# Optimization experiments

Measured on AMD Instinct MI355X. Metric: run time of the kernel, lower is better.

The kernel has to match this reference:

```python
import jax, jax.numpy as jnp
import numpy as np


def setup_inputs() -> dict:
    key = jax.random.key(0)
    B, S, D, H = 4, 2048, 1024, 16
    hd = D // H
    ks = jax.random.split(key, 11)
    sc = 1.0 / np.sqrt(D)
    return {
        "keys": jax.random.normal(ks[0], (B, S, D), jnp.float32),
        "queries": jax.random.normal(ks[1], (B, S, D), jnp.float32),
        "values": jax.random.normal(ks[2], (B, S, D), jnp.float32),
        "Wq": jax.random.normal(ks[3], (H, D, hd), jnp.float32) * sc,
        "bq": jax.random.normal(ks[4], (H, hd), jnp.float32) * 0.02,
        "Wk": jax.random.normal(ks[5], (H, D, hd), jnp.float32) * sc,
        "bk": jax.random.normal(ks[6], (H, hd), jnp.float32) * 0.02,
        "Wv": jax.random.normal(ks[7], (H, D, hd), jnp.float32) * sc,
        "bv": jax.random.normal(ks[8], (H, hd), jnp.float32) * 0.02,
        "Wo": jax.random.normal(ks[9], (D, D), jnp.float32) * sc,
        "bo": jax.random.normal(ks[10], (D,), jnp.float32) * 0.02,
    }


def reference(keys, queries, values, Wq, bq, Wk, bk, Wv, bv, Wo, bo):
    # Per-head linear projections: [B,S,D] x [H,D,hd] -> [B,H,S,hd]
    q = jnp.einsum("bsd,hde->bhse", queries, Wq) + bq[None, :, None, :]
    k = jnp.einsum("bsd,hde->bhse", keys, Wk) + bk[None, :, None, :]
    v = jnp.einsum("bsd,hde->bhse", values, Wv) + bv[None, :, None, :]

    hd = q.shape[-1]
    S = q.shape[2]
    scores = jnp.einsum("bhse,bhte->bhst", q, k) / jnp.sqrt(jnp.float32(hd))
    causal = jnp.tril(jnp.ones((S, S), dtype=bool))  # tril buffer
    scores = jnp.where(causal[None, None, :, :], scores, -jnp.inf)
    attn = jax.nn.softmax(scores, axis=-1)  # dropout p=0 (eval)

    o = jnp.einsum("bhst,bhte->bhse", attn, v)  # [B,H,S,hd]
    # concat heads -> [B,S,H*hd]
    o = o.transpose(0, 2, 1, 3).reshape(o.shape[0], S, -1)
    return o @ Wo + bo
```

## Files before the change

### kernel.cpp

```cpp
#include <hip/hip_runtime.h>
#include <stdint.h>

typedef unsigned short u16;
typedef __attribute__((ext_vector_type(4))) float f32x4;
typedef __attribute__((ext_vector_type(8))) short bfrag;

static __device__ __forceinline__ u16 f2bf(float f) {
  union { float f; uint32_t u; } v; v.f = f;
  return (u16)((v.u + 0x7fffu + ((v.u >> 16) & 1u)) >> 16);
}
static __device__ __forceinline__ uint32_t cvtpk(float lo, float hi) {
  uint32_t r;
  asm("v_cvt_pk_bf16_f32 %0, %1, %2" : "=v"(r) : "v"(lo), "v"(hi));
  return r;
}
static __device__ __forceinline__ uint32_t pk2bf(float lo, float hi) {
  union { float f; uint32_t u; } a, b; a.f = lo; b.f = hi;
  return __builtin_amdgcn_perm(b.u + 0x8000u, a.u + 0x8000u, 0x07060302u);
}

#define GLOAD16(gp, lp)                                              \
  __builtin_amdgcn_global_load_lds(                                  \
      (const __attribute__((address_space(1))) uint32_t*)(gp),       \
      (__attribute__((address_space(3))) uint32_t*)(lp), 16, 0, 0)

__global__ __launch_bounds__(256) void pack_w_hde(const float* __restrict__ W,
                                                  u16* __restrict__ Wt) {
  __shared__ float tile[64][65];
  const int h = blockIdx.y, k0 = blockIdx.x * 64;
  const int tid = threadIdx.x;
#pragma unroll
  for (int j = 0; j < 4; ++j) {
    int idx = tid + j * 256;
    int rr = idx >> 4, c4 = (idx & 15) * 4;
    const float4 v = *(const float4*)(W + (size_t)h * 65536 + (size_t)(k0 + rr) * 64 + c4);
    tile[rr][c4 + 0] = v.x; tile[rr][c4 + 1] = v.y;
    tile[rr][c4 + 2] = v.z; tile[rr][c4 + 3] = v.w;
  }
  __syncthreads();
#pragma unroll
  for (int j = 0; j < 4; ++j) {
    int idx = tid + j * 256;
    int ee = idx >> 4, c4 = (idx & 15) * 4;
    uint2 u;
    u.x = f2bf(tile[c4 + 0][ee]) | ((uint32_t)f2bf(tile[c4 + 1][ee]) << 16);
    u.y = f2bf(tile[c4 + 2][ee]) | ((uint32_t)f2bf(tile[c4 + 3][ee]) << 16);
    *(uint2*)(Wt + (size_t)(h * 64 + ee) * 1024 + k0 + c4) = u;
  }
}

__global__ __launch_bounds__(256) void transpose_w(const float* __restrict__ W,
                                                   u16* __restrict__ Wt) {
  __shared__ float tile[64][65];
  const int k0 = blockIdx.x * 64, n0 = blockIdx.y * 64;
  const int tid = threadIdx.x;
#pragma unroll
  for (int j = 0; j < 4; ++j) {
    int idx = tid + j * 256;
    int rr = idx >> 4, c4 = (idx & 15) * 4;
    const float4 v = *(const float4*)(W + (size_t)(k0 + rr) * 1024 + n0 + c4);
    tile[rr][c4 + 0] = v.x; tile[rr][c4 + 1] = v.y;
    tile[rr][c4 + 2] = v.z; tile[rr][c4 + 3] = v.w;
  }
  __syncthreads();
#pragma unroll
  for (int j = 0; j < 4; ++j) {
    int idx = tid + j * 256;
    int ee = idx >> 4, c4 = (idx & 15) * 4;
    uint2 u;
    u.x = f2bf(tile[c4 + 0][ee]) | ((uint32_t)f2bf(tile[c4 + 1][ee]) << 16);
    u.y = f2bf(tile[c4 + 2][ee]) | ((uint32_t)f2bf(tile[c4 + 3][ee]) << 16);
    *(uint2*)(Wt + (size_t)(n0 + ee) * 1024 + k0 + c4) = u;
  }
}

__global__ __launch_bounds__(256) void conv_bf16(const float* __restrict__ q,
                                                 const float* __restrict__ k,
                                                 const float* __restrict__ v,
                                                 u16* __restrict__ oq,
                                                 u16* __restrict__ ok,
                                                 u16* __restrict__ ov) {
  const float* in = (blockIdx.y == 0) ? q : (blockIdx.y == 1) ? k : v;
  u16* out = (blockIdx.y == 0) ? oq : (blockIdx.y == 1) ? ok : ov;
  const size_t i = ((size_t)blockIdx.x * 256 + threadIdx.x) * 8;
  const float4 f0 = *(const float4*)(in + i);
  const float4 f1 = *(const float4*)(in + i + 4);
  uint4 u;
  u.x = pk2bf(f0.x, f0.y); u.y = pk2bf(f0.z, f0.w);
  u.z = pk2bf(f1.x, f1.y); u.w = pk2bf(f1.z, f1.w);
  *(uint4*)(out + i) = u;
}

__global__ __launch_bounds__(256) void gemm_qkvb(
    const u16* __restrict__ cq, const u16* __restrict__ ck,
    const u16* __restrict__ cv, const u16* __restrict__ Bt,
    const float* __restrict__ bq, const float* __restrict__ bk,
    const float* __restrict__ bv,
    u16* __restrict__ Qb, u16* __restrict__ Kb, u16* __restrict__ Vt) {
  __shared__ u16 As[2][128 * 32];
  __shared__ u16 Bs[2][128 * 32];
  const int tid = threadIdx.x;
  const int n = blockIdx.x;
  const int xcd = n & 7, j = n >> 3;
  const int mb = xcd * 8 + (j & 7);
  const int nb = j >> 3;
  const int chunk = nb >> 3;
  const u16* Abf = (chunk == 0) ? cq : (chunk == 1) ? ck : cv;
  const int wid = tid >> 6, lane = tid & 63;
  const int wr = wid >> 1, wc = wid & 1;
  const int g = lane >> 4, l15 = lane & 15;
  f32x4 acc[4][4] = {};

  const int bsrc = ((lane & 3) ^ ((lane >> 3) & 3)) * 8;
  const int swzr = (l15 >> 1) & 3;
  const u16* Bg = Bt + (size_t)(nb * 128 + 2 * wid * 16 + (lane >> 2)) * 1024 + bsrc;
  const u16* Ag = Abf + (size_t)(mb * 128 + 2 * wid * 16 + (lane >> 2)) * 1024 + bsrc;

#pragma unroll
  for (int c = 0; c < 2; ++c) {
    GLOAD16(Ag + (size_t)c * 16 * 1024, &As[0][2 * wid * 512 + c * 512]);
    GLOAD16(Bg + (size_t)c * 16 * 1024, &Bs[0][2 * wid * 512 + c * 512]);
  }
  __syncthreads();
  int cur = 0;
  for (int kk = 0; kk < 32; ++kk) {
    if (kk < 31) {
      const int kn = (kk + 1) * 32;
#pragma unroll
      for (int c = 0; c < 2; ++c) {
        GLOAD16(Ag + (size_t)c * 16 * 1024 + kn, &As[cur ^ 1][2 * wid * 512 + c * 512]);
        GLOAD16(Bg + (size_t)c * 16 * 1024 + kn, &Bs[cur ^ 1][2 * wid * 512 + c * 512]);
      }
    }
    bfrag a[4], b[4];
#pragma unroll
    for (int m = 0; m < 4; ++m)
      a[m] = __builtin_bit_cast(bfrag,
          *(const uint4*)&As[cur][(wr * 64 + m * 16 + l15) * 32 + ((g ^ swzr)) * 8]);
#pragma unroll
    for (int nn = 0; nn < 4; ++nn)
      b[nn] = __builtin_bit_cast(bfrag,
          *(const uint4*)&Bs[cur][(wc * 64 + nn * 16 + l15) * 32 + ((g ^ swzr)) * 8]);
    __builtin_amdgcn_s_setprio(1);
#pragma unroll
    for (int m = 0; m < 4; ++m)
#pragma unroll
      for (int nn = 0; nn < 4; ++nn)
        acc[m][nn] = __builtin_amdgcn_mfma_f32_16x16x32_bf16(a[m], b[nn], acc[m][nn], 0, 0, 0);
    __builtin_amdgcn_s_setprio(0);
    if (kk < 31) { __syncthreads(); cur ^= 1; }
  }

  const int row0 = mb * 128 + wr * 64 + g * 4;
  const int cc0 = (nb & 7) * 128 + wc * 64 + l15;
  const float* bias = (chunk == 0) ? bq : (chunk == 1) ? bk : bv;
  const float qs = (chunk == 0) ? 0.125f : 1.0f;
#pragma unroll
  for (int m = 0; m < 4; ++m) {
#pragma unroll
    for (int nn = 0; nn < 4; ++nn) {
      const int row = row0 + m * 16;
      const int cc = cc0 + nn * 16;
      const float bcv = bias[cc];
      if (chunk < 2) {
        u16* dst = (chunk == 0) ? Qb : Kb;
#pragma unroll
        for (int r = 0; r < 4; ++r)
          dst[(size_t)(row + r) * 1024 + cc] = f2bf((acc[m][nn][r] + bcv) * qs);
      } else {
        u16 w[4];
#pragma unroll
        for (int r = 0; r < 4; ++r) w[r] = f2bf(acc[m][nn][r] + bcv);
        const size_t dst =
            ((size_t)((row >> 11) * 16 + (cc >> 6)) * 64 + (cc & 63)) * 2048 + (row & 2047);
        *(uint2*)(Vt + dst) = *(const uint2*)w;
      }
    }
  }
}

__global__ __launch_bounds__(256) void gemm_qkv(
    const float* __restrict__ Aq, const float* __restrict__ Ak,
    const float* __restrict__ Avv, const u16* __restrict__ Bt,
    const float* __restrict__ bq, const float* __restrict__ bk,
    const float* __restrict__ bv,
    u16* __restrict__ Qb, u16* __restrict__ Kb, u16* __restrict__ Vt) {
  __shared__ u16 As[2][128 * 32];
  __shared__ u16 Bs[2][128 * 32];
  const int tid = threadIdx.x;
  const int n = blockIdx.x;
  const int xcd = n & 7, j = n >> 3;
  const int mb = xcd * 8 + (j & 7);
  const int nb = j >> 3;
  const int chunk = nb >> 3;
  const float* Af = (chunk == 0) ? Aq : (chunk == 1) ? Ak : Avv;
  const int wid = tid >> 6, lane = tid & 63;
  const int wr = wid >> 1, wc = wid & 1;
  const int g = lane >> 4, l15 = lane & 15;
  f32x4 acc[4][4] = {};

  const int bsrc = ((lane & 3) ^ ((lane >> 3) & 3)) * 8;
  const u16* Bg = Bt + (size_t)(nb * 128 + 2 * wid * 16 + (lane >> 2)) * 1024 + bsrc;
  const float* Ap = Af + (size_t)(mb * 128 + (tid >> 2)) * 1024 + (tid & 3) * 8;
  const int arow = tid >> 2;
  const int acs = (((tid & 3) ^ ((tid >> 3) & 3))) * 8;
  const int swzr = (l15 >> 1) & 3;

  float4 fa[2][2];
#pragma unroll
  for (int c = 0; c < 2; ++c) {
    fa[c][0] = *(const float4*)(Ap + (size_t)c * 64 * 1024);
    fa[c][1] = *(const float4*)(Ap + (size_t)c * 64 * 1024 + 4);
  }
#pragma unroll
  for (int c = 0; c < 2; ++c)
    GLOAD16(Bg + (size_t)c * 16 * 1024, &Bs[0][2 * wid * 512 + c * 512]);
#pragma unroll
  for (int c = 0; c < 2; ++c) {
    uint4 u;
    u.x = pk2bf(fa[c][0].x, fa[c][0].y); u.y = pk2bf(fa[c][0].z, fa[c][0].w);
    u.z = pk2bf(fa[c][1].x, fa[c][1].y); u.w = pk2bf(fa[c][1].z, fa[c][1].w);
    *(uint4*)&As[0][(arow + c * 64) * 32 + acs] = u;
  }
  __syncthreads();
  int cur = 0;
  for (int kk = 0; kk < 32; ++kk) {
    if (kk < 31) {
      const int kn = (kk + 1) * 32;
#pragma unroll
      for (int c = 0; c < 2; ++c) {
        fa[c][0] = *(const float4*)(Ap + (size_t)c * 64 * 1024 + kn);
        fa[c][1] = *(const float4*)(Ap + (size_t)c * 64 * 1024 + kn + 4);
      }
#pragma unroll
      for (int c = 0; c < 2; ++c)
        GLOAD16(Bg + (size_t)c * 16 * 1024 + kn, &Bs[cur ^ 1][2 * wid * 512 + c * 512]);
    }
    bfrag a[4], b[4];
#pragma unroll
    for (int m = 0; m < 4; ++m)
      a[m] = __builtin_bit_cast(bfrag,
          *(const uint4*)&As[cur][(wr * 64 + m * 16 + l15) * 32 + ((g ^ swzr)) * 8]);
#pragma unroll
    for (int nn = 0; nn < 4; ++nn)
      b[nn] = __builtin_bit_cast(bfrag,
          *(const uint4*)&Bs[cur][(wc * 64 + nn * 16 + l15) * 32 + ((g ^ swzr)) * 8]);
    __builtin_amdgcn_s_setprio(1);
#pragma unroll
    for (int m = 0; m < 4; ++m)
#pragma unroll
      for (int nn = 0; nn < 4; ++nn)
        acc[m][nn] = __builtin_amdgcn_mfma_f32_16x16x32_bf16(a[m], b[nn], acc[m][nn], 0, 0, 0);
    __builtin_amdgcn_s_setprio(0);
    if (kk < 31) {
#pragma unroll
      for (int c = 0; c < 2; ++c) {
        uint4 u;
        u.x = pk2bf(fa[c][0].x, fa[c][0].y); u.y = pk2bf(fa[c][0].z, fa[c][0].w);
        u.z = pk2bf(fa[c][1].x, fa[c][1].y); u.w = pk2bf(fa[c][1].z, fa[c][1].w);
        *(uint4*)&As[cur ^ 1][(arow + c * 64) * 32 + acs] = u;
      }
      __syncthreads();
      cur ^= 1;
    }
  }

  const int row0 = mb * 128 + wr * 64 + g * 4;
  const int cc0 = (nb & 7) * 128 + wc * 64 + l15;
  const float* bias = (chunk == 0) ? bq : (chunk == 1) ? bk : bv;
  const float qs = (chunk == 0) ? 0.125f : 1.0f;
#pragma unroll
  for (int m = 0; m < 4; ++m) {
#pragma unroll
    for (int nn = 0; nn < 4; ++nn) {
      const int row = row0 + m * 16;
      const int cc = cc0 + nn * 16;
      const float bcv = bias[cc];
      if (chunk < 2) {
        u16* dst = (chunk == 0) ? Qb : Kb;
#pragma unroll
        for (int r = 0; r < 4; ++r)
          dst[(size_t)(row + r) * 1024 + cc] = f2bf((acc[m][nn][r] + bcv) * qs);
      } else {
        u16 w[4];
#pragma unroll
        for (int r = 0; r < 4; ++r) w[r] = f2bf(acc[m][nn][r] + bcv);
        const size_t dst =
            ((size_t)((row >> 11) * 16 + (cc >> 6)) * 64 + (cc & 63)) * 2048 + (row & 2047);
        *(uint2*)(Vt + dst) = *(const uint2*)w;
      }
    }
  }
}

__global__ __launch_bounds__(256) void gemm_o(const u16* __restrict__ Abf,
                                              const u16* __restrict__ Bt,
                                              const float* __restrict__ bo,
                                              float* __restrict__ Of) {
  __shared__ u16 As[2][128 * 32];
  __shared__ u16 Bs[2][128 * 32];
  const int tid = threadIdx.x;
  const int n = blockIdx.x;
  const int xcd = n & 7, j = n >> 3;
  const int mb = xcd * 8 + (j & 7);
  const int nb = j >> 3;
  const int wid = tid >> 6, lane = tid & 63;
  const int wr = wid >> 1, wc = wid & 1;
  const int g = lane >> 4, l15 = lane & 15;
  f32x4 acc[4][4] = {};

  const int bsrc = ((lane & 3) ^ ((lane >> 3) & 3)) * 8;
  const int swzr = (l15 >> 1) & 3;
  const u16* Bg = Bt + (size_t)(nb * 128 + 2 * wid * 16 + (lane >> 2)) * 1024 + bsrc;
  const u16* Ag = Abf + (size_t)(mb * 128 + 2 * wid * 16 + (lane >> 2)) * 1024 + bsrc;

#pragma unroll
  for (int c = 0; c < 2; ++c) {
    GLOAD16(Ag + (size_t)c * 16 * 1024, &As[0][2 * wid * 512 + c * 512]);
    GLOAD16(Bg + (size_t)c * 16 * 1024, &Bs[0][2 * wid * 512 + c * 512]);
  }
  __syncthreads();
  int cur = 0;
  for (int kk = 0; kk < 32; ++kk) {
    if (kk < 31) {
      const int kn = (kk + 1) * 32;
#pragma unroll
      for (int c = 0; c < 2; ++c) {
        GLOAD16(Ag + (size_t)c * 16 * 1024 + kn, &As[cur ^ 1][2 * wid * 512 + c * 512]);
        GLOAD16(Bg + (size_t)c * 16 * 1024 + kn, &Bs[cur ^ 1][2 * wid * 512 + c * 512]);
      }
    }
    bfrag a[4], b[4];
#pragma unroll
    for (int m = 0; m < 4; ++m)
      a[m] = __builtin_bit_cast(bfrag,
          *(const uint4*)&As[cur][(wr * 64 + m * 16 + l15) * 32 + ((g ^ swzr)) * 8]);
#pragma unroll
    for (int nn = 0; nn < 4; ++nn)
      b[nn] = __builtin_bit_cast(bfrag,
          *(const uint4*)&Bs[cur][(wc * 64 + nn * 16 + l15) * 32 + ((g ^ swzr)) * 8]);
    __builtin_amdgcn_s_setprio(1);
#pragma unroll
    for (int m = 0; m < 4; ++m)
#pragma unroll
      for (int nn = 0; nn < 4; ++nn)
        acc[m][nn] = __builtin_amdgcn_mfma_f32_16x16x32_bf16(a[m], b[nn], acc[m][nn], 0, 0, 0);
    __builtin_amdgcn_s_setprio(0);
    if (kk < 31) { __syncthreads(); cur ^= 1; }
  }

  const int row0 = mb * 128 + wr * 64 + g * 4;
  const int col0 = nb * 128 + wc * 64 + l15;
#pragma unroll
  for (int m = 0; m < 4; ++m)
#pragma unroll
    for (int nn = 0; nn < 4; ++nn) {
      const int row = row0 + m * 16, col = col0 + nn * 16;
      const float bcv = bo[col];
#pragma unroll
      for (int r = 0; r < 4; ++r)
        Of[(size_t)(row + r) * 1024 + col] = acc[m][nn][r] + bcv;
    }
}

__global__ __launch_bounds__(512) void attn_fused(const u16* __restrict__ Qb,
                                                  const u16* __restrict__ Kb,
                                                  const u16* __restrict__ Vtg,
                                                  u16* __restrict__ Ob) {
  __shared__ u16 KV[2][2][4096];
  const int tid = threadIdx.x;
  const int wid = tid >> 6, lane = tid & 63;
  const int g = lane >> 4, l15 = lane & 15;
  const int n = blockIdx.x;
  const int half = n >> 8, idx = n & 255;
  const int xcd = idx & 7;
  const int bh = xcd * 8 + ((idx >> 3) & 7);
  const int grp = idx >> 6;
  const int u = half ? grp : (7 - grp);
  const int t = u * 8 + wid;
  const int b = bh >> 4, h = bh & 15;
  const size_t baserow = (size_t)b * 2048;
  const u16* Qg = Qb + baserow * 1024 + h * 64;
  const u16* Kg = Kb + baserow * 1024 + h * 64;
  const u16* Vg = Vtg + (size_t)bh * 64 * 2048;
  u16* Og = Ob + baserow * 1024 + h * 64;

  const int q0 = t * 32;
  const int qrow = q0 + l15;
  const int mysteps = (q0 >> 6) + 1;
  const int smax = 4 * u + 4;

  const int sr = tid >> 3;
  const int scc = (tid & 7) ^ (sr & 7);
  const u16* Kst = Kg + (size_t)sr * 1024 + scc * 8;
  const u16* Vst = Vg + (size_t)sr * 2048 + scc * 8;

  bfrag qa[2][2];
#pragma unroll
  for (int qf = 0; qf < 2; ++qf)
#pragma unroll
    for (int kh = 0; kh < 2; ++kh)
      qa[qf][kh] = __builtin_bit_cast(bfrag,
          *(const uint4*)(Qg + (size_t)(q0 + qf * 16 + l15) * 1024 + kh * 32 + g * 8));

  f32x4 accT[2][4] = {};
  float M[2] = {-1e30f, -1e30f}, Ll[2] = {0.f, 0.f};

  const int s0lane = ((g & 1) << 5) | l15;
  const int s1lane = s0lane + 16;
  const bool ghi = (g >= 2);
  const int swz = l15 & 7;

  GLOAD16(Kst, &KV[0][0][wid * 512]);
  GLOAD16(Vst, &KV[0][1][wid * 512]);
  __syncthreads();

  for (int s = 0; s < smax; ++s) {
    const int cb = s & 1;
    if (s + 1 < smax) {
      const size_t kn = (size_t)(s + 1) << 6;
      GLOAD16(Kst + kn * 1024, &KV[cb ^ 1][0][wid * 512]);
      GLOAD16(Vst + kn, &KV[cb ^ 1][1][wid * 512]);
    }
    if (s < mysteps) {
      const int kv0 = s << 6;
      const bool diag = (s == mysteps - 1);
      const u16* KB = &KV[cb][0][0];
      const u16* VB = &KV[cb][1][0];

      bfrag kb[2][4];
#pragma unroll
      for (int tt = 0; tt < 4; ++tt)
#pragma unroll
        for (int kh = 0; kh < 2; ++kh)
          kb[kh][tt] = __builtin_bit_cast(bfrag,
              *(const uint4*)&KB[(tt * 16 + l15) * 64 + (((kh << 2) | g) ^ swz) * 8]);

      f32x4 sc[2][4];
      __builtin_amdgcn_s_setprio(1);
#pragma unroll
      for (int qf = 0; qf < 2; ++qf)
#pragma unroll
        for (int tt = 0; tt < 4; ++tt) {
          f32x4 z = {0.f, 0.f, 0.f, 0.f};
          z = __builtin_amdgcn_mfma_f32_16x16x32_bf16(kb[0][tt], qa[qf][0], z, 0, 0, 0);
          z = __builtin_amdgcn_mfma_f32_16x16x32_bf16(kb[1][tt], qa[qf][1], z, 0, 0, 0);
          sc[qf][tt] = z;
        }
      __builtin_amdgcn_s_setprio(0);

      bfrag vb[2][4];
#pragma unroll
      for (int et = 0; et < 4; ++et)
#pragma unroll
        for (int kcb = 0; kcb < 2; ++kcb)
          vb[kcb][et] = __builtin_bit_cast(bfrag,
              *(const uint4*)&VB[(et * 16 + l15) * 64 + (((kcb << 2) | g) ^ swz) * 8]);

#pragma unroll
      for (int qf = 0; qf < 2; ++qf) {
        if (diag) {
          const int qq = qrow + qf * 16;
#pragma unroll
          for (int tt = 0; tt < 4; ++tt) {
            const int kvb = kv0 + tt * 16 + g * 4;
#pragma unroll
            for (int r = 0; r < 4; ++r)
              sc[qf][tt][r] = (kvb + r <= qq) ? sc[qf][tt][r] : -1e30f;
          }
        }
        float m01 = fmaxf(fmaxf(sc[qf][0][0], sc[qf][0][1]), fmaxf(sc[qf][0][2], sc[qf][0][3]));
        float m23 = fmaxf(fmaxf(sc[qf][1][0], sc[qf][1][1]), fmaxf(sc[qf][1][2], sc[qf][1][3]));
        float m45 = fmaxf(fmaxf(sc[qf][2][0], sc[qf][2][1]), fmaxf(sc[qf][2][2], sc[qf][2][3]));
        float m67 = fmaxf(fmaxf(sc[qf][3][0], sc[qf][3][1]), fmaxf(sc[qf][3][2], sc[qf][3][3]));
        const float mloc = fmaxf(fmaxf(m01, m23), fmaxf(m45, m67));
        if (!__all(mloc - M[qf] <= 6.0f)) {
          float mr = fmaxf(mloc, __shfl_xor(mloc, 16));
          mr = fmaxf(mr, __shfl_xor(mr, 32));
          const float Mn = fmaxf(M[qf], mr);
          const float cf = __expf(M[qf] - Mn);
          M[qf] = Mn;
          Ll[qf] *= cf;
#pragma unroll
          for (int et = 0; et < 4; ++et)
#pragma unroll
            for (int r = 0; r < 4; ++r) accT[qf][et][r] *= cf;
        }
        uint32_t pk[4][2];
        float ss = 0.f;
#pragma unroll
        for (int tt = 0; tt < 4; ++tt) {
          float p0 = __expf(sc[qf][tt][0] - M[qf]);
          float p1 = __expf(sc[qf][tt][1] - M[qf]);
          float p2 = __expf(sc[qf][tt][2] - M[qf]);
          float p3 = __expf(sc[qf][tt][3] - M[qf]);
          ss += (p0 + p1) + (p2 + p3);
          pk[tt][0] = cvtpk(p0, p1);
          pk[tt][1] = cvtpk(p2, p3);
        }
        Ll[qf] += ss;
        __builtin_amdgcn_s_setprio(1);
#pragma unroll
        for (int kcb = 0; kcb < 2; ++kcb) {
          const int lo = kcb * 2, hi = kcb * 2 + 1;
          const uint32_t a0 = __shfl(pk[lo][0], s0lane), b0 = __shfl(pk[hi][0], s0lane);
          const uint32_t a1 = __shfl(pk[lo][1], s0lane), b1 = __shfl(pk[hi][1], s0lane);
          const uint32_t a2 = __shfl(pk[lo][0], s1lane), b2 = __shfl(pk[hi][0], s1lane);
          const uint32_t a3 = __shfl(pk[lo][1], s1lane), b3 = __shfl(pk[hi][1], s1lane);
          uint4 uu;
          uu.x = ghi ? b0 : a0; uu.y = ghi ? b1 : a1;
          uu.z = ghi ? b2 : a2; uu.w = ghi ? b3 : a3;
          const bfrag pfrag = __builtin_bit_cast(bfrag, uu);
#pragma unroll
          for (int et = 0; et < 4; ++et)
            accT[qf][et] = __builtin_amdgcn_mfma_f32_16x16x32_bf16(vb[kcb][et], pfrag, accT[qf][et], 0, 0, 0);
        }
        __builtin_amdgcn_s_setprio(0);
      }
    }
    __syncthreads();
  }

#pragma unroll
  for (int qf = 0; qf < 2; ++qf) {
    float Ls = Ll[qf];
    Ls += __shfl_xor(Ls, 16);
    Ls += __shfl_xor(Ls, 32);
    const float inv = 1.f / Ls;
    u16* orow = Og + (size_t)(q0 + qf * 16 + l15) * 1024 + g * 4;
#pragma unroll
    for (int et = 0; et < 4; ++et) {
      uint2 w;
      w.x = cvtpk(accT[qf][et][0] * inv, accT[qf][et][1] * inv);
      w.y = cvtpk(accT[qf][et][2] * inv, accT[qf][et][3] * inv);
      *(uint2*)(orow + et * 16) = w;
    }
  }
}

extern "C" void kernel_launch(void* const* d_in, const int* in_sizes, int n_in,
                              void* d_out, int out_size, void* d_ws, size_t ws_size,
                              hipStream_t stream) {
  const float* keys    = (const float*)d_in[0];
  const float* queries = (const float*)d_in[1];
  const float* values  = (const float*)d_in[2];
  const float* Wq = (const float*)d_in[3];
  const float* bq = (const float*)d_in[4];
  const float* Wk = (const float*)d_in[5];
  const float* bk = (const float*)d_in[6];
  const float* Wv = (const float*)d_in[7];
  const float* bv = (const float*)d_in[8];
  const float* Wo = (const float*)d_in[9];
  const float* bo = (const float*)d_in[10];
  float* out = (float*)d_out;

  char* ws = (char*)d_ws;
  const size_t MB = 1u << 20;
  u16* Wqkvt = (u16*)(ws);
  u16* Wot   = (u16*)(ws + 6 * MB);
  u16* Qb    = (u16*)(ws + 8 * MB);
  u16* Kb    = (u16*)(ws + 24 * MB);
  u16* Vtg   = (u16*)(ws + 40 * MB);
  u16* Ob    = (u16*)(ws + 56 * MB);
  u16* cvQ   = (u16*)(ws + 56 * MB);
  u16* cvK   = (u16*)(ws + 72 * MB);
  u16* cvV   = (u16*)(ws + 88 * MB);

  const dim3 pg(16, 16);
  pack_w_hde<<<pg, 256, 0, stream>>>(Wq, Wqkvt);
  pack_w_hde<<<pg, 256, 0, stream>>>(Wk, Wqkvt + (size_t)1024 * 1024);
  pack_w_hde<<<pg, 256, 0, stream>>>(Wv, Wqkvt + (size_t)2048 * 1024);
  transpose_w<<<pg, 256, 0, stream>>>(Wo, Wot);

  if (ws_size >= 104 * MB) {
    conv_bf16<<<dim3(4096, 3), 256, 0, stream>>>(queries, keys, values, cvQ, cvK, cvV);
    gemm_qkvb<<<dim3(1536), 256, 0, stream>>>(cvQ, cvK, cvV, Wqkvt,
                                              bq, bk, bv, Qb, Kb, Vtg);
  } else {
    gemm_qkv<<<dim3(1536), 256, 0, stream>>>(queries, keys, values, Wqkvt,
                                             bq, bk, bv, Qb, Kb, Vtg);
  }

  attn_fused<<<dim3(512), 512, 0, stream>>>(Qb, Kb, Vtg, Ob);

  gemm_o<<<dim3(512), 256, 0, stream>>>(Ob, Wot, bo, out);
}
```

Before: 208.7 us.

## Use 256x256 tiles with 8 waves in QKV projection GEMM

Replaces the 128x128, 4-wave QKV GEMM with a 256x256-tile, 8-wave (512-thread) kernel using K-steps of 64. Next-tile loads are split across four sub-phases interleaved with the MFMA groups, and barriers separate the phases. Larger tiles raise arithmetic intensity and cut global/L2 traffic per flop. In exchange the block count drops to 384, 128 accumulator floats per thread raise register pressure, and there are more barriers per K step.

```diff
diff --git a/kernel.cpp b/kernel.cpp
--- a/kernel.cpp
+++ b/kernel.cpp
@@ -91,92 +91,118 @@
   *(uint4*)(out + i) = u;
 }
 
-__global__ __launch_bounds__(256) void gemm_qkvb(
+__global__ __launch_bounds__(512, 2) void gemm_qkvb8(
     const u16* __restrict__ cq, const u16* __restrict__ ck,
     const u16* __restrict__ cv, const u16* __restrict__ Bt,
     const float* __restrict__ bq, const float* __restrict__ bk,
     const float* __restrict__ bv,
     u16* __restrict__ Qb, u16* __restrict__ Kb, u16* __restrict__ Vt) {
-  __shared__ u16 As[2][128 * 32];
-  __shared__ u16 Bs[2][128 * 32];
+  __shared__ u16 Ab[2][2][8192];
+  __shared__ u16 Bb[2][2][8192];
   const int tid = threadIdx.x;
+  const int wid = tid >> 6, lane = tid & 63;
+  const int wr = wid >> 2, wc = wid & 3;
+  const int g = lane >> 4, l15 = lane & 15;
   const int n = blockIdx.x;
   const int xcd = n & 7, j = n >> 3;
-  const int mb = xcd * 8 + (j & 7);
-  const int nb = j >> 3;
-  const int chunk = nb >> 3;
+  const int mb = xcd * 4 + (j & 3);
+  const int nb = j >> 2;
+  const int chunk = nb >> 2, nbl = nb & 3;
   const u16* Abf = (chunk == 0) ? cq : (chunk == 1) ? ck : cv;
-  const int wid = tid >> 6, lane = tid & 63;
-  const int wr = wid >> 1, wc = wid & 1;
-  const int g = lane >> 4, l15 = lane & 15;
-  f32x4 acc[4][4] = {};
-
-  const int bsrc = ((lane & 3) ^ ((lane >> 3) & 3)) * 8;
-  const int swzr = (l15 >> 1) & 3;
-  const u16* Bg = Bt + (size_t)(nb * 128 + 2 * wid * 16 + (lane >> 2)) * 1024 + bsrc;
-  const u16* Ag = Abf + (size_t)(mb * 128 + 2 * wid * 16 + (lane >> 2)) * 1024 + bsrc;
-
-#pragma unroll
-  for (int c = 0; c < 2; ++c) {
-    GLOAD16(Ag + (size_t)c * 16 * 1024, &As[0][2 * wid * 512 + c * 512]);
-    GLOAD16(Bg + (size_t)c * 16 * 1024, &Bs[0][2 * wid * 512 + c * 512]);
-  }
-  __syncthreads();
-  int cur = 0;
-  for (int kk = 0; kk < 32; ++kk) {
-    if (kk < 31) {
-      const int kn = (kk + 1) * 32;
-#pragma unroll
-      for (int c = 0; c < 2; ++c) {
-        GLOAD16(Ag + (size_t)c * 16 * 1024 + kn, &As[cur ^ 1][2 * wid * 512 + c * 512]);
-        GLOAD16(Bg + (size_t)c * 16 * 1024 + kn, &Bs[cur ^ 1][2 * wid * 512 + c * 512]);
-      }
-    }
-    bfrag a[4], b[4];
-#pragma unroll
-    for (int m = 0; m < 4; ++m)
-      a[m] = __builtin_bit_cast(bfrag,
-          *(const uint4*)&As[cur][(wr * 64 + m * 16 + l15) * 32 + ((g ^ swzr)) * 8]);
-#pragma unroll
-    for (int nn = 0; nn < 4; ++nn)
-      b[nn] = __builtin_bit_cast(bfrag,
-          *(const uint4*)&Bs[cur][(wc * 64 + nn * 16 + l15) * 32 + ((g ^ swzr)) * 8]);
-    __builtin_amdgcn_s_setprio(1);
-#pragma unroll
-    for (int m = 0; m < 4; ++m)
-#pragma unroll
-      for (int nn = 0; nn < 4; ++nn)
-        acc[m][nn] = __builtin_amdgcn_mfma_f32_16x16x32_bf16(a[m], b[nn], acc[m][nn], 0, 0, 0);
-    __builtin_amdgcn_s_setprio(0);
-    if (kk < 31) { __syncthreads(); cur ^= 1; }
-  }
-
-  const int row0 = mb * 128 + wr * 64 + g * 4;
-  const int cc0 = (nb & 7) * 128 + wc * 64 + l15;
+
+  const int srow = tid >> 3;
+  const int schk = (tid & 7) ^ (srow & 7);
+  const u16* Ag = Abf + (size_t)(mb * 256 + srow) * 1024 + schk * 8;
+  const u16* Bg = Bt + (size_t)(nb * 256 + srow) * 1024 + schk * 8;
+
+  f32x4 acc[8][4] = {};
+
+#define STG_A(db, hf, kt) {                                                  \
+    GLOAD16(Ag + ((size_t)(hf)*128) * 1024 + (kt) * 64, &Ab[db][hf][tid * 8]); \
+    GLOAD16(Ag + ((size_t)(hf)*128 + 64) * 1024 + (kt) * 64,                 \
+            &Ab[db][hf][4096 + tid * 8]); }
+#define STG_B(db, hf, kt) {                                                  \
+    GLOAD16(Bg + ((size_t)(hf)*128) * 1024 + (kt) * 64, &Bb[db][hf][tid * 8]); \
+    GLOAD16(Bg + ((size_t)(hf)*128 + 64) * 1024 + (kt) * 64,                 \
+            &Bb[db][hf][4096 + tid * 8]); }
+
+  STG_A(0, 0, 0) STG_A(0, 1, 0) STG_B(0, 0, 0) STG_B(0, 1, 0)
+  asm volatile("s_waitcnt vmcnt(0)" ::: "memory");
+  __builtin_amdgcn_s_barrier();
+
+  const int swz = l15 & 7;
+  for (int kt = 0; kt < 16; ++kt) {
+    const int db = kt & 1, dn = db ^ 1;
+    bfrag bfr[2][4], afr[2][2];
+#pragma unroll
+    for (int mq = 0; mq < 4; ++mq) {
+      if (mq == 0) {
+#pragma unroll
+        for (int nf = 0; nf < 4; ++nf)
+#pragma unroll
+          for (int ks = 0; ks < 2; ++ks)
+            bfr[ks][nf] = __builtin_bit_cast(bfrag,
+                *(const uint4*)&Bb[db][wc >> 1]
+                    [((wc & 1) * 64 + nf * 16 + l15) * 64 + ((ks * 4 + g) ^ swz) * 8]);
+      }
+#pragma unroll
+      for (int m2 = 0; m2 < 2; ++m2)
+#pragma unroll
+        for (int ks = 0; ks < 2; ++ks)
+          afr[ks][m2] = __builtin_bit_cast(bfrag,
+              *(const uint4*)&Ab[db][wr]
+                  [((mq * 2 + m2) * 16 + l15) * 64 + ((ks * 4 + g) ^ swz) * 8]);
+      if (kt < 15) {
+        if (mq == 0)      STG_A(dn, 0, kt + 1)
+        else if (mq == 1) STG_A(dn, 1, kt + 1)
+        else if (mq == 2) STG_B(dn, 0, kt + 1)
+        else              STG_B(dn, 1, kt + 1)
+      }
+      __builtin_amdgcn_s_barrier();
+      __builtin_amdgcn_s_setprio(1);
+#pragma unroll
+      for (int m2 = 0; m2 < 2; ++m2)
+#pragma unroll
+        for (int nf = 0; nf < 4; ++nf) {
+          acc[mq * 2 + m2][nf] = __builtin_amdgcn_mfma_f32_16x16x32_bf16(
+              afr[0][m2], bfr[0][nf], acc[mq * 2 + m2][nf], 0, 0, 0);
+          acc[mq * 2 + m2][nf] = __builtin_amdgcn_mfma_f32_16x16x32_bf16(
+              afr[1][m2], bfr[1][nf], acc[mq * 2 + m2][nf], 0, 0, 0);
+        }
+      __builtin_amdgcn_s_setprio(0);
+      if (mq == 3) asm volatile("s_waitcnt vmcnt(0)" ::: "memory");
+      __builtin_amdgcn_s_barrier();
+    }
+  }
+
+  const int row0 = mb * 256 + wr * 128 + g * 4;
+  const int cc0 = nbl * 256 + wc * 64 + l15;
   const float* bias = (chunk == 0) ? bq : (chunk == 1) ? bk : bv;
   const float qs = (chunk == 0) ? 0.125f : 1.0f;
 #pragma unroll
-  for (int m = 0; m < 4; ++m) {
-#pragma unroll
-    for (int nn = 0; nn < 4; ++nn) {
-      const int row = row0 + m * 16;
-      const int cc = cc0 + nn * 16;
+  for (int mf = 0; mf < 8; ++mf) {
+#pragma unroll
+    for (int nf = 0; nf < 4; ++nf) {
+      const int row = row0 + mf * 16;
+      const int cc = cc0 + nf * 16;
       const float bcv = bias[cc];
       if (chunk < 2) {
         u16* dst = (chunk == 0) ? Qb : Kb;
 #pragma unroll
         for (int r = 0; r < 4; ++r)
-          dst[(size_t)(row + r) * 1024 + cc] = f2bf((acc[m][nn][r] + bcv) * qs);
+          dst[(size_t)(row + r) * 1024 + cc] = f2bf((acc[mf][nf][r] + bcv) * qs);
       } else {
         u16 w[4];
 #pragma unroll
-        for (int r = 0; r < 4; ++r) w[r] = f2bf(acc[m][nn][r] + bcv);
+        for (int r = 0; r < 4; ++r) w[r] = f2bf(acc[mf][nf][r] + bcv);
         const size_t dst =
             ((size_t)((row >> 11) * 16 + (cc >> 6)) * 64 + (cc & 63)) * 2048 + (row & 2047);
         *(uint2*)(Vt + dst) = *(const uint2*)w;
       }
     }
   }
+#undef STG_A
+#undef STG_B
 }
 
 __global__ __launch_bounds__(256) void gemm_qkv(
@@ -574,7 +600,7 @@
 
   if (ws_size >= 104 * MB) {
     conv_bf16<<<dim3(4096, 3), 256, 0, stream>>>(queries, keys, values, cvQ, cvK, cvV);
-    gemm_qkvb<<<dim3(1536), 256, 0, stream>>>(cvQ, cvK, cvV, Wqkvt,
+    gemm_qkvb8<<<dim3(384), 512, 0, stream>>>(cvQ, cvK, cvV, Wqkvt,
                                               bq, bk, bv, Qb, Kb, Vtg);
   } else {
     gemm_qkv<<<dim3(1536), 256, 0, stream>>>(queries, keys, values, Wqkvt,
```

New measurement: 213.1 us. 2.1% more time.
